# Kernel optimization log

Hardware: AMD Instinct MI355X
Metric: run time of the kernel (lower is better)

Reference implementation:

```python
import jax, jax.numpy as jnp
import numpy as np

TEMPERATURE = 0.07
EPS = 1e-6  # arccosh domain clamp: argument must be >= 1


def setup_inputs() -> dict:
    key = jax.random.key(0)
    k1, k2 = jax.random.split(key)
    N, D = 8192, 768
    v_hyp = jax.random.normal(k1, (N, D), dtype=jnp.float32)
    t_hyp = jax.random.normal(k2, (N, D), dtype=jnp.float32)
    c = jnp.float32(1.0)  # curvature (positive scalar)
    return {"v_hyp": v_hyp, "t_hyp": t_hyp, "c": c}


def _pairwise_hyperbolic_dist(v, t, c):
    # Lorentz/hyperboloid pairwise distance with curvature c:
    #   x_time = sqrt(1/c + ||x||^2)
    #   <x,y>_L = x . y - x_time * y_time
    #   d(x,y) = (1/sqrt(c)) * arccosh(clamp(-c * <x,y>_L, min=1+eps))
    inv_c = 1.0 / c
    v_time = jnp.sqrt(inv_c + jnp.sum(v * v, axis=-1))  # [N]
    t_time = jnp.sqrt(inv_c + jnp.sum(t * t, axis=-1))  # [N]
    lorentz = jnp.einsum("nd,md->nm", v, t) - v_time[:, None] * t_time[None, :]
    arg = jnp.maximum(-c * lorentz, 1.0 + EPS)
    return jnp.sqrt(inv_c) * jnp.arccosh(arg)  # [N, N]


def _ce_diag(logits):
    # cross-entropy with labels = arange(N), mean reduction
    logp = jax.nn.log_softmax(logits, axis=-1)
    return -jnp.mean(jnp.diagonal(logp))


def reference(v_hyp, t_hyp, c):
    dist = _pairwise_hyperbolic_dist(v_hyp, t_hyp, c)
    logits = -dist / TEMPERATURE  # [N, N]
    loss_v2t = _ce_diag(logits)
    loss_t2v = _ce_diag(logits.T)
    return (loss_v2t + loss_t2v) * 0.5
```

## Files before the change

### kernel.cpp

```cpp
#include <hip/hip_runtime.h>
#include <hip/hip_bf16.h>
#include <math.h>

#define NROWS 8192
#define DDIM  768
#define TEMP_INV 14.285714285714286f
#define EPSX 1e-6f
#define NKT  12
#define SHIFT 55.0f
#define SHIFT_E 79.34282475f
#define QS   20.0f
#define SLOT 16384
#define PLANE ((size_t)NROWS * 64)
#define LROW 784

typedef __attribute__((ext_vector_type(4))) int   i32x4;
typedef unsigned int   u32;

#define GLOAD16(gaddr, laddr)                                                   \
  __builtin_amdgcn_global_load_lds(                                             \
      (const __attribute__((address_space(1))) u32*)(gaddr),                    \
      (__attribute__((address_space(3))) u32*)(laddr), 16, 0, 0)

#define MFMAI8(a,b,c) __builtin_amdgcn_mfma_i32_16x16x64_i8((a),(b),(c),0,0,0)

__device__ __forceinline__ u32 q8(float x){
  int q = __float2int_rn(x * QS);
  q = q < -127 ? -127 : (q > 127 ? 127 : q);
  return (u32)(q & 255);
}

template<int CTRL>
__device__ __forceinline__ float dpp_rot_add(float v){
  int r = __builtin_amdgcn_update_dpp(0, __float_as_int(v), CTRL, 0xF, 0xF, true);
  return v + __int_as_float(r);
}
__device__ __forceinline__ float row_sum16(float v){
  v = dpp_rot_add<0x121>(v);
  v = dpp_rot_add<0x122>(v);
  v = dpp_rot_add<0x124>(v);
  v = dpp_rot_add<0x128>(v);
  return v;
}

__global__ __launch_bounds__(256) void prep_kernel(
    const float* __restrict__ v, const float* __restrict__ t, const float* __restrict__ cptr,
    char* __restrict__ vp, char* __restrict__ tp,
    float* __restrict__ vtime, float* __restrict__ ttime, float* __restrict__ diag)
{
  __shared__ char ldsv[16*LROW];
  __shared__ char ldst[16*LROW];
  const int tid = threadIdx.x;
  const int lane = tid & 63, wid = tid >> 6;
  const int row0 = blockIdx.x * 16;
  const float inv_c = 1.0f / cptr[0];

  #pragma unroll
  for (int it = 0; it < 4; it++){
    const int r   = wid*4 + it;
    const int row = row0 + r;
    const float4* vr = (const float4*)(v + (size_t)row * DDIM);
    const float4* tr = (const float4*)(t + (size_t)row * DDIM);
    const int sw = (r >> 1) & 3;
    float sv = 0.f, st = 0.f, dd = 0.f;
    #pragma unroll
    for (int j = 0; j < 3; j++){
      const int k4 = lane + j*64;
      float4 a = vr[k4], b = tr[k4];
      sv += a.x*a.x + a.y*a.y + a.z*a.z + a.w*a.w;
      st += b.x*b.x + b.y*b.y + b.z*b.z + b.w*b.w;
      dd += a.x*b.x + a.y*b.y + a.z*b.z + a.w*b.w;
      const u32 pv = q8(a.x) | (q8(a.y)<<8) | (q8(a.z)<<16) | (q8(a.w)<<24);
      const u32 pt = q8(b.x) | (q8(b.y)<<8) | (q8(b.z)<<16) | (q8(b.w)<<24);
      const int kt = k4 >> 4;
      const int cc = ((k4 >> 2) & 3) ^ sw;
      const int off = r*LROW + kt*64 + cc*16 + (k4 & 3)*4;
      *(u32*)(ldsv + off) = pv;
      *(u32*)(ldst + off) = pt;
    }
    #pragma unroll
    for (int o = 32; o; o >>= 1){
      sv += __shfl_down(sv, o);
      st += __shfl_down(st, o);
      dd += __shfl_down(dd, o);
    }
    if (!lane){
      vtime[row] = sqrtf(inv_c + sv);
      ttime[row] = sqrtf(inv_c + st);
      diag[row]  = dd;
    }
  }
  __syncthreads();

  #pragma unroll
  for (int j = 0; j < 3; j++){
    const int idx = j*256 + tid;
    const int kt = idx >> 6, s = idx & 63, r = s >> 2, cc = s & 3;
    const size_t g = (size_t)kt*PLANE + (size_t)(row0 + r)*64 + cc*16;
    const int l = r*LROW + kt*64 + cc*16;
    *(i32x4*)(vp + g) = *(const i32x4*)(ldsv + l);
    *(i32x4*)(tp + g) = *(const i32x4*)(ldst + l);
  }
}

__global__ __launch_bounds__(512, 6) void tile_kernel(
    const char* __restrict__ vp, const char* __restrict__ tp,
    const float* __restrict__ vtime, const float* __restrict__ ttime,
    const float* __restrict__ cptr,
    float* __restrict__ rowPsum, float* __restrict__ colPsum)
{
  __shared__ char SMc[3*SLOT];
  __shared__ float vtl2[128], ttl[128];

  const int tid = threadIdx.x;
  const int lane = tid & 63, wid = tid >> 6;
  const int wm = wid >> 1, wn = wid & 1;
  const int lo = lane & 15, hi = lane >> 4;

  const float c = cptr[0];
  const float c2 = c + c;
  const float slog = -(1.0f/sqrtf(c)) * TEMP_INV;
  const float wmin = c2 * (1.0f + EPSX);
  const float kq   = c2 * (1.0f/(QS*QS));

  const int linear = blockIdx.x;
  const int xcd = linear & 7, s = linear >> 3;
  const int xr = xcd & 1, xc = xcd >> 1;
  const int by = xr*32 + (s & 3) + ((s >> 6) << 2);
  const int bx = xc*16 + ((s >> 2) & 15);

  if (tid < 128){ vtl2[tid] = c2 * vtime[by*128 + tid]; }
  else if (tid < 256){ ttl[tid-128] = ttime[bx*128 + tid - 128]; }

  const char* pA0 = vp + ((size_t)(by*128 + (wid<<4)) << 6) + (lane << 4);
  const char* pB0 = tp + ((size_t)(bx*128 + (wid<<4)) << 6) + (lane << 4);
  const int dA = wid*1024;
  const int dB = 8192 + wid*1024;

  const int swb  = (hi ^ ((lo >> 1) & 3)) * 16;
  const int arow = (wm*32 + lo) * 64 + swb;
  const int brow = 8192 + (wn*64 + lo) * 64 + swb;

  i32x4 acc[2][4];
  #pragma unroll
  for (int m = 0; m < 2; m++)
    #pragma unroll
    for (int n = 0; n < 4; n++)
      acc[m][n] = (i32x4){0,0,0,0};

#define STG(kt) do{                                                              \
    char* s_ = SMc + ((kt) % 3) * SLOT;                                          \
    GLOAD16(pA0 + (size_t)(kt)*PLANE, s_ + dA);                                  \
    GLOAD16(pB0 + (size_t)(kt)*PLANE, s_ + dB); }while(0)

  STG(0); STG(1);
  asm volatile("s_waitcnt vmcnt(2) lgkmcnt(0)" ::: "memory");
  __builtin_amdgcn_s_barrier();

  #pragma unroll
  for (int t = 0; t < NKT; t++){
    __builtin_amdgcn_sched_barrier(0);
    const char* S = SMc + (t % 3) * SLOT;
    if (t + 2 < NKT) STG(t + 2);
    i32x4 b[4];
    #pragma unroll
    for (int n = 0; n < 4; n++) b[n] = *(const i32x4*)(S + brow + n*1024);
    i32x4 a0 = *(const i32x4*)(S + arow);
    i32x4 a1 = *(const i32x4*)(S + arow + 1024);
    __builtin_amdgcn_s_setprio(1);
    #pragma unroll
    for (int n = 0; n < 4; n++){
      acc[0][n] = MFMAI8(a0, b[n], acc[0][n]);
      acc[1][n] = MFMAI8(a1, b[n], acc[1][n]);
    }
    __builtin_amdgcn_s_setprio(0);
    if (t < NKT-2)       asm volatile("s_waitcnt vmcnt(2) lgkmcnt(0)" ::: "memory");
    else if (t == NKT-2) asm volatile("s_waitcnt vmcnt(0) lgkmcnt(0)" ::: "memory");
    else                 asm volatile("s_waitcnt lgkmcnt(0)" ::: "memory");
    __builtin_amdgcn_s_barrier();
  }
#undef STG

  __syncthreads();

  #pragma unroll
  for (int m = 0; m < 2; m++){
    #pragma unroll
    for (int n = 0; n < 4; n++){
      #pragma unroll
      for (int q = 0; q < 4; q++){
        int r  = wm*32 + m*16 + hi*4 + q;
        int cc = wn*64 + n*16 + lo;
        float w = fmaf(-kq, (float)acc[m][n][q], vtl2[r] * ttl[cc]);
        w = fmaxf(w, wmin);
        acc[m][n][q] = __float_as_int(exp2f(fmaf(slog, log2f(w), SHIFT_E)));
      }
    }
  }

  float* reds  = (float*)SMc;
  float* redcs = reds + 256;

  #pragma unroll
  for (int m = 0; m < 2; m++){
    #pragma unroll
    for (int q = 0; q < 4; q++){
      float s2 = (__int_as_float(acc[m][0][q]) + __int_as_float(acc[m][1][q]))
               + (__int_as_float(acc[m][2][q]) + __int_as_float(acc[m][3][q]));
      s2 = row_sum16(s2);
      if (lo == 0)
        reds[wn*128 + wm*32 + m*16 + hi*4 + q] = s2;
    }
  }
  __syncthreads();
  if (tid < 128){
    float S = reds[tid] + reds[128 + tid];
    rowPsum[(size_t)bx*NROWS + by*128 + tid] = S;
  }

  #pragma unroll
  for (int n = 0; n < 4; n++){
    float s2 = 0.f;
    #pragma unroll
    for (int m = 0; m < 2; m++)
      #pragma unroll
      for (int q = 0; q < 4; q++) s2 += __int_as_float(acc[m][n][q]);
    s2 += __shfl_xor(s2, 16);
    s2 += __shfl_xor(s2, 32);
    if (hi == 0)
      redcs[wm*128 + wn*64 + n*16 + lo] = s2;
  }
  __syncthreads();
  if (tid < 128){
    float S = (redcs[tid] + redcs[128 + tid]) + (redcs[256 + tid] + redcs[384 + tid]);
    colPsum[(size_t)by*NROWS + bx*128 + tid] = S;
  }
}

__global__ __launch_bounds__(256) void lse_reduce(
    const float* __restrict__ rowPsum, const float* __restrict__ colPsum,
    float* __restrict__ psums)
{
  const int i = blockIdx.x * 256 + threadIdx.x;
  const float* Ps = blockIdx.y ? colPsum : rowPsum;
  float S = 0.f;
  for (int b = 0; b < 64; b++)
    S += Ps[(size_t)b*NROWS + i];
  float lse = __logf(S) - SHIFT;
  for (int o = 32; o; o >>= 1) lse += __shfl_down(lse, o);
  __shared__ float red[4];
  int lane = threadIdx.x & 63, wid = threadIdx.x >> 6;
  if (!lane) red[wid] = lse;
  __syncthreads();
  if (!threadIdx.x)
    psums[blockIdx.y*32 + blockIdx.x] = red[0]+red[1]+red[2]+red[3];
}

__global__ __launch_bounds__(1024) void final_kernel(
    const float* __restrict__ psums, const float* __restrict__ vtime,
    const float* __restrict__ ttime, const float* __restrict__ diag,
    const float* __restrict__ cptr, float* __restrict__ out)
{
  int tid = threadIdx.x;
  float c = cptr[0];
  float slog = -(1.0f/sqrtf(c)) * TEMP_INV;
  float dsum = 0.f;
  #pragma unroll
  for (int it = 0; it < 8; it++){
    int i = tid + it*1024;
    float arg = c * (vtime[i]*ttime[i] - diag[i]);
    arg = fmaxf(arg, 1.0f + EPSX);
    dsum += slog * __logf(arg + sqrtf(arg*arg - 1.0f));
  }
  for (int o = 32; o; o >>= 1) dsum += __shfl_down(dsum, o);
  __shared__ float red[16];
  if (!(tid & 63)) red[tid >> 6] = dsum;
  __syncthreads();
  if (tid < 64){
    float p = psums[tid];
    for (int o = 32; o; o >>= 1) p += __shfl_down(p, o);
    if (!tid){
      float dtot = 0.f;
      #pragma unroll
      for (int k = 0; k < 16; k++) dtot += red[k];
      out[0] = 0.5f*p/NROWS - dtot/NROWS;
    }
  }
}

extern "C" void kernel_launch(void* const* d_in, const int* in_sizes, int n_in,
                              void* d_out, int out_size, void* d_ws, size_t ws_size,
                              hipStream_t stream) {
  const float* v = (const float*)d_in[0];
  const float* t = (const float*)d_in[1];
  const float* c = (const float*)d_in[2];

  char* ws = (char*)d_ws;
  const size_t NB = (size_t)NROWS * DDIM;
  char*  vp      = ws;
  char*  tp      = ws + NB;
  float* vtime   = (float*)(ws + 2*NB);
  float* ttime   = (float*)(ws + 2*NB + NROWS*4);
  float* diag    = (float*)(ws + 2*NB + 2*(size_t)NROWS*4);
  char*  p       = ws + 2*NB + 3*(size_t)NROWS*4;
  float* rowPsum = (float*)(p);
  float* colPsum = (float*)(p + (size_t)64*NROWS*4);
  float* psums   = (float*)(p + (size_t)128*NROWS*4);

  prep_kernel<<<512, 256, 0, stream>>>(v, t, c, vp, tp, vtime, ttime, diag);
  tile_kernel<<<4096, 512, 0, stream>>>(vp, tp, vtime, ttime, c, rowPsum, colPsum);
  lse_reduce<<<dim3(32, 2), 256, 0, stream>>>(rowPsum, colPsum, psums);
  final_kernel<<<1, 1024, 0, stream>>>(psums, vtime, ttime, diag, c, (float*)d_out);
}
```

Baseline: 102.6 us.

## Use 4 waves per block with larger per-wave MFMA tiles

Halves the tile kernel's block to 256 threads (4 waves, 2x2 layout). Each wave now computes a 64x64 sub-tile, with 16 accumulators instead of 8 and two global-to-LDS loads per operand per stage. The goal is more MFMA reuse per LDS fragment load and fewer waves synchronizing at each barrier. The trade-off is higher register pressure and lower occupancy (launch bounds 3 blocks per CU), so there are fewer waves to hide latency.

```diff
diff --git a/kernel.cpp b/kernel.cpp
--- a/kernel.cpp
+++ b/kernel.cpp
@@ -103,7 +103,7 @@
   }
 }
 
-__global__ __launch_bounds__(512, 6) void tile_kernel(
+__global__ __launch_bounds__(256, 3) void tile_kernel(
     const char* __restrict__ vp, const char* __restrict__ tp,
     const float* __restrict__ vtime, const float* __restrict__ ttime,
     const float* __restrict__ cptr,
@@ -130,31 +130,34 @@
   const int bx = xc*16 + ((s >> 2) & 15);
 
   if (tid < 128){ vtl2[tid] = c2 * vtime[by*128 + tid]; }
-  else if (tid < 256){ ttl[tid-128] = ttime[bx*128 + tid - 128]; }
-
-  const char* pA0 = vp + ((size_t)(by*128 + (wid<<4)) << 6) + (lane << 4);
-  const char* pB0 = tp + ((size_t)(bx*128 + (wid<<4)) << 6) + (lane << 4);
-  const int dA = wid*1024;
-  const int dB = 8192 + wid*1024;
+  else          { ttl[tid-128] = ttime[bx*128 + tid - 128]; }
+
+  const int dl0 = wid*1024;
+  const int dl1 = 4096 + wid*1024;
+  const char* gA = vp + ((size_t)by << 13) + dl0 + (lane << 4);
+  const char* gB = tp + ((size_t)bx << 13) + dl0 + (lane << 4);
 
   const int swb  = (hi ^ ((lo >> 1) & 3)) * 16;
-  const int arow = (wm*32 + lo) * 64 + swb;
+  const int arow = (wm*64 + lo) * 64 + swb;
   const int brow = 8192 + (wn*64 + lo) * 64 + swb;
 
-  i32x4 acc[2][4];
-  #pragma unroll
-  for (int m = 0; m < 2; m++)
+  i32x4 acc[4][4];
+  #pragma unroll
+  for (int m = 0; m < 4; m++)
     #pragma unroll
     for (int n = 0; n < 4; n++)
       acc[m][n] = (i32x4){0,0,0,0};
 
 #define STG(kt) do{                                                              \
     char* s_ = SMc + ((kt) % 3) * SLOT;                                          \
-    GLOAD16(pA0 + (size_t)(kt)*PLANE, s_ + dA);                                  \
-    GLOAD16(pB0 + (size_t)(kt)*PLANE, s_ + dB); }while(0)
+    const size_t p_ = (size_t)(kt) * PLANE;                                      \
+    GLOAD16(gA + p_,        s_ + dl0);                                           \
+    GLOAD16(gA + p_ + 4096, s_ + dl1);                                           \
+    GLOAD16(gB + p_,        s_ + 8192 + dl0);                                    \
+    GLOAD16(gB + p_ + 4096, s_ + 8192 + dl1); }while(0)
 
   STG(0); STG(1);
-  asm volatile("s_waitcnt vmcnt(2) lgkmcnt(0)" ::: "memory");
+  asm volatile("s_waitcnt vmcnt(4) lgkmcnt(0)" ::: "memory");
   __builtin_amdgcn_s_barrier();
 
   #pragma unroll
@@ -162,19 +165,19 @@
     __builtin_amdgcn_sched_barrier(0);
     const char* S = SMc + (t % 3) * SLOT;
     if (t + 2 < NKT) STG(t + 2);
-    i32x4 b[4];
+    i32x4 b[4], a[4];
     #pragma unroll
     for (int n = 0; n < 4; n++) b[n] = *(const i32x4*)(S + brow + n*1024);
-    i32x4 a0 = *(const i32x4*)(S + arow);
-    i32x4 a1 = *(const i32x4*)(S + arow + 1024);
+    #pragma unroll
+    for (int m = 0; m < 4; m++) a[m] = *(const i32x4*)(S + arow + m*1024);
     __builtin_amdgcn_s_setprio(1);
     #pragma unroll
-    for (int n = 0; n < 4; n++){
-      acc[0][n] = MFMAI8(a0, b[n], acc[0][n]);
-      acc[1][n] = MFMAI8(a1, b[n], acc[1][n]);
-    }
+    for (int m = 0; m < 4; m++)
+      #pragma unroll
+      for (int n = 0; n < 4; n++)
+        acc[m][n] = MFMAI8(a[m], b[n], acc[m][n]);
     __builtin_amdgcn_s_setprio(0);
-    if (t < NKT-2)       asm volatile("s_waitcnt vmcnt(2) lgkmcnt(0)" ::: "memory");
+    if (t < NKT-2)       asm volatile("s_waitcnt vmcnt(4) lgkmcnt(0)" ::: "memory");
     else if (t == NKT-2) asm volatile("s_waitcnt vmcnt(0) lgkmcnt(0)" ::: "memory");
     else                 asm volatile("s_waitcnt lgkmcnt(0)" ::: "memory");
     __builtin_amdgcn_s_barrier();
@@ -184,12 +187,12 @@
   __syncthreads();
 
   #pragma unroll
-  for (int m = 0; m < 2; m++){
+  for (int m = 0; m < 4; m++){
     #pragma unroll
     for (int n = 0; n < 4; n++){
       #pragma unroll
       for (int q = 0; q < 4; q++){
-        int r  = wm*32 + m*16 + hi*4 + q;
+        int r  = wm*64 + m*16 + hi*4 + q;
         int cc = wn*64 + n*16 + lo;
         float w = fmaf(-kq, (float)acc[m][n][q], vtl2[r] * ttl[cc]);
         w = fmaxf(w, wmin);
@@ -202,14 +205,14 @@
   float* redcs = reds + 256;
 
   #pragma unroll
-  for (int m = 0; m < 2; m++){
+  for (int m = 0; m < 4; m++){
     #pragma unroll
     for (int q = 0; q < 4; q++){
       float s2 = (__int_as_float(acc[m][0][q]) + __int_as_float(acc[m][1][q]))
                + (__int_as_float(acc[m][2][q]) + __int_as_float(acc[m][3][q]));
       s2 = row_sum16(s2);
       if (lo == 0)
-        reds[wn*128 + wm*32 + m*16 + hi*4 + q] = s2;
+        reds[wn*128 + wm*64 + m*16 + hi*4 + q] = s2;
     }
   }
   __syncthreads();
@@ -222,7 +225,7 @@
   for (int n = 0; n < 4; n++){
     float s2 = 0.f;
     #pragma unroll
-    for (int m = 0; m < 2; m++)
+    for (int m = 0; m < 4; m++)
       #pragma unroll
       for (int q = 0; q < 4; q++) s2 += __int_as_float(acc[m][n][q]);
     s2 += __shfl_xor(s2, 16);
@@ -232,7 +235,7 @@
   }
   __syncthreads();
   if (tid < 128){
-    float S = (redcs[tid] + redcs[128 + tid]) + (redcs[256 + tid] + redcs[384 + tid]);
+    float S = redcs[tid] + redcs[128 + tid];
     colPsum[(size_t)by*NROWS + bx*128 + tid] = S;
   }
 }
@@ -308,7 +311,7 @@
   float* psums   = (float*)(p + (size_t)128*NROWS*4);
 
   prep_kernel<<<512, 256, 0, stream>>>(v, t, c, vp, tp, vtime, ttime, diag);
-  tile_kernel<<<4096, 512, 0, stream>>>(vp, tp, vtime, ttime, c, rowPsum, colPsum);
+  tile_kernel<<<4096, 256, 0, stream>>>(vp, tp, vtime, ttime, c, rowPsum, colPsum);
   lse_reduce<<<dim3(32, 2), 256, 0, stream>>>(rowPsum, colPsum, psums);
   final_kernel<<<1, 1024, 0, stream>>>(psums, vtime, ttime, diag, c, (float*)d_out);
 }
```

Result: no change. 101.9 us (median of 2 runs) (-0.7%).
